# Optimization experiments

Hardware: AMD Instinct MI355X
Metric: run time of the kernel (lower is better)

Reference implementation:

```python
import jax, jax.numpy as jnp
import numpy as np

N_NODES = 100000
N_EDGES = 1600000
NUM_FEATURES = 128
HIDDEN = 128


def _linear_init(key, fan_in, fan_out):
    kw, kb = jax.random.split(key)
    bound = 1.0 / np.sqrt(fan_in)
    w = jax.random.uniform(kw, (fan_in, fan_out), jnp.float32, -bound, bound)
    b = jax.random.uniform(kb, (fan_out,), jnp.float32, -bound, bound)
    return w, b


def setup_inputs() -> dict:
    key = jax.random.key(0)
    ks = jax.random.split(key, 8)
    x = jax.random.normal(ks[0], (N_NODES, NUM_FEATURES), jnp.float32)
    edge_index = jax.random.randint(ks[1], (2, N_EDGES), 0, N_NODES, jnp.int64)
    w11, b11 = _linear_init(ks[2], NUM_FEATURES, HIDDEN)
    w12, b12 = _linear_init(ks[3], HIDDEN, HIDDEN)
    w21, b21 = _linear_init(ks[4], HIDDEN, HIDDEN)
    w22, b22 = _linear_init(ks[5], HIDDEN, HIDDEN)
    w31, b31 = _linear_init(ks[6], HIDDEN, HIDDEN)
    w32, b32 = _linear_init(ks[7], HIDDEN, 1)
    return {"x": x, "edge_index": edge_index,
            "w11": w11, "b11": b11, "w12": w12, "b12": b12,
            "w21": w21, "b21": b21, "w22": w22, "b22": b22,
            "w31": w31, "b31": b31, "w32": w32, "b32": b32}


def _gin_conv(x, src, dst, w1, b1, w2, b2):
    # GINConv (eps=0): h_i = MLP(x_i + sum_{j->i} x_j)
    agg = jax.ops.segment_sum(x[src], dst, num_segments=N_NODES)
    h = x + agg
    h = jax.nn.relu(h @ w1 + b1)
    return h @ w2 + b2


def reference(x, edge_index, w11, b11, w12, b12, w21, b21, w22, b22, w31, b31, w32, b32):
    src, dst = edge_index[0], edge_index[1]
    h = _gin_conv(x, src, dst, w11, b11, w12, b12)
    h = _gin_conv(h, src, dst, w21, b21, w22, b22)
    h = _gin_conv(h, src, dst, w31, b31, w32, b32)  # [N, 1]
    return h
```

## Files before the change

### kernel.cpp

```cpp
#include <hip/hip_runtime.h>

#define NN 100000
#define NE 1600000
#define F 128
#define NBUCK ((NN + 255) >> 8)
#define SCAT_BLOCKS 512
#define EPB (NE / SCAT_BLOCKS)
#define IDX_CAP 1536

typedef _Float16 f16x8 __attribute__((ext_vector_type(8)));
typedef float    f32x4 __attribute__((ext_vector_type(4)));
typedef unsigned short ushort8v __attribute__((ext_vector_type(8)));
typedef unsigned short ushort4v __attribute__((ext_vector_type(4)));

__device__ inline unsigned short f2h(float f) {
    _Float16 h = (_Float16)f;
    return __builtin_bit_cast(unsigned short, h);
}
__device__ inline float h2f(unsigned short u) {
    return (float)__builtin_bit_cast(_Float16, u);
}

__global__ __launch_bounds__(256) void k_bhist(const int* __restrict__ dst, int* __restrict__ bcnt) {
    __shared__ int sc[NBUCK];
    for (int i = threadIdx.x; i < NBUCK; i += 256) sc[i] = 0;
    __syncthreads();
    int stride = gridDim.x * 256;
    for (int e = blockIdx.x * 256 + threadIdx.x; e < NE; e += stride)
        atomicAdd(&sc[dst[e] >> 8], 1);
    __syncthreads();
    for (int i = threadIdx.x; i < NBUCK; i += 256) {
        int c = sc[i];
        if (c) atomicAdd(&bcnt[i], c);
    }
}

__global__ void k_bscan(const int* __restrict__ bcnt, int* __restrict__ bbase, int* __restrict__ bcur) {
    __shared__ int s[512];
    int t = threadIdx.x;
    int v = (t < NBUCK) ? bcnt[t] : 0;
    s[t] = v;
    __syncthreads();
    for (int off = 1; off < 512; off <<= 1) {
        int u = (t >= off) ? s[t - off] : 0;
        __syncthreads();
        s[t] += u;
        __syncthreads();
    }
    int excl = s[t] - v;
    if (t < NBUCK) { bbase[t] = excl; bcur[t] = excl; }
    if (t == 0) bbase[NBUCK] = NE;
}

__global__ __launch_bounds__(256) void k_scatterA(const int* __restrict__ src,
                                                  const int* __restrict__ dst,
                                                  int* __restrict__ bcur,
                                                  unsigned* __restrict__ scratch) {
    __shared__ uint2 sEdge[EPB];
    __shared__ int cnt[512];
    __shared__ int scn[512];
    __shared__ int cntB[512];
    __shared__ int gbase[512];
    __shared__ int ssum[256];

    const int tid = threadIdx.x;
    const int ebase = blockIdx.x * EPB;

#pragma unroll
    for (int i = tid; i < 512; i += 256) { cnt[i] = 0; cntB[i] = 0; }
    __syncthreads();

    for (int i = tid; i < EPB; i += 256) {
        int b = dst[ebase + i] >> 8;
        atomicAdd(&cnt[b], 1);
    }
    __syncthreads();

    int c0 = cnt[2 * tid], c1 = cnt[2 * tid + 1];
    ssum[tid] = c0 + c1;
    __syncthreads();
    for (int off = 1; off < 256; off <<= 1) {
        int v = (tid >= off) ? ssum[tid - off] : 0;
        __syncthreads();
        ssum[tid] += v;
        __syncthreads();
    }
    int texcl = (tid == 0) ? 0 : ssum[tid - 1];
    scn[2 * tid] = texcl;
    scn[2 * tid + 1] = texcl + c0;
#pragma unroll
    for (int i = tid; i < NBUCK; i += 256) {
        int c = cnt[i];
        gbase[i] = c ? atomicAdd(&bcur[i], c) : 0;
    }
    __syncthreads();

    for (int i = tid; i < EPB; i += 256) {
        int s = src[ebase + i], d = dst[ebase + i];
        int b = d >> 8;
        int rank = atomicAdd(&cntB[b], 1);
        sEdge[scn[b] + rank] = make_uint2((unsigned)s, (unsigned)d);
    }
    __syncthreads();

    for (int i = tid; i < EPB; i += 256) {
        uint2 ed = sEdge[i];
        int b = (int)(ed.y >> 8);
        unsigned w = ((ed.y & 255u) << 24) | ed.x;
        scratch[gbase[b] + (i - scn[b])] = w;
    }
}

__global__ __launch_bounds__(256) void k_fillB(const int* __restrict__ bbase,
                                               const unsigned* __restrict__ scratch,
                                               int* __restrict__ row_ptr,
                                               int* __restrict__ csr) {
    __shared__ int cnt[256];
    __shared__ int s[256];
    __shared__ int cur[256];
    int b = blockIdx.x;
    int base = bbase[b], end = bbase[b + 1];
    int t = threadIdx.x;
    cnt[t] = 0;
    __syncthreads();
    for (int i = base + t; i < end; i += 256)
        atomicAdd(&cnt[scratch[i] >> 24], 1);
    __syncthreads();
    int v = cnt[t];
    s[t] = v;
    __syncthreads();
    for (int off = 1; off < 256; off <<= 1) {
        int u = (t >= off) ? s[t - off] : 0;
        __syncthreads();
        s[t] += u;
        __syncthreads();
    }
    int excl = s[t] - v;
    int node = (b << 8) + t;
    if (node < NN) row_ptr[node] = base + excl;
    if (b == NBUCK - 1 && t == 0) row_ptr[NN] = NE;
    cur[t] = excl;
    __syncthreads();
    for (int i = base + t; i < end; i += 256) {
        unsigned w = scratch[i];
        int n = w >> 24;
        int p = atomicAdd(&cur[n], 1);
        csr[base + p] = (int)(w & 0xFFFFFFu);
    }
}

__global__ void k_x2h(const float* __restrict__ x, unsigned short* __restrict__ xh) {
    int idx = blockIdx.x * 256 + threadIdx.x;
    float4 v = ((const float4*)x)[idx];
    ushort4v h;
    h.x = f2h(v.x);
    h.y = f2h(v.y);
    h.z = f2h(v.z);
    h.w = f2h(v.w);
    ((ushort4v*)xh)[idx] = h;
}

struct WPack {
    const float* w[5];
    unsigned short* t[5];
};

__global__ void k_w2h(WPack p) {
    int which = blockIdx.x >> 6;
    int idx = (blockIdx.x & 63) * 256 + threadIdx.x;
    int n = idx >> 7, k = idx & 127;
    p.t[which][idx] = f2h(p.w[which][k * 128 + n]);
}

template <bool LOC>
__device__ __forceinline__ void accum_rows(float a[8], int st, int e,
                                           const int* __restrict__ sIdx,
                                           const int* __restrict__ gIdx,
                                           const unsigned short* __restrict__ G,
                                           int lofs) {
    int p = st;
    for (; p + 8 <= e; p += 8) {
        int j[8];
#pragma unroll
        for (int q = 0; q < 8; ++q) j[q] = LOC ? sIdx[p + q] : gIdx[p + q];
        ushort8v v[8];
#pragma unroll
        for (int q = 0; q < 8; ++q) v[q] = *(const ushort8v*)&G[(size_t)j[q] * F + lofs];
#pragma unroll
        for (int k = 0; k < 8; ++k) {
            float t0 = (h2f(v[0][k]) + h2f(v[1][k])) + (h2f(v[2][k]) + h2f(v[3][k]));
            float t1 = (h2f(v[4][k]) + h2f(v[5][k])) + (h2f(v[6][k]) + h2f(v[7][k]));
            a[k] += t0 + t1;
        }
    }
    if (p + 4 <= e) {
        int j[4];
#pragma unroll
        for (int q = 0; q < 4; ++q) j[q] = LOC ? sIdx[p + q] : gIdx[p + q];
        ushort8v v[4];
#pragma unroll
        for (int q = 0; q < 4; ++q) v[q] = *(const ushort8v*)&G[(size_t)j[q] * F + lofs];
#pragma unroll
        for (int k = 0; k < 8; ++k)
            a[k] += (h2f(v[0][k]) + h2f(v[1][k])) + (h2f(v[2][k]) + h2f(v[3][k]));
        p += 4;
    }
    if (p + 2 <= e) {
        int j0 = LOC ? sIdx[p] : gIdx[p];
        int j1 = LOC ? sIdx[p + 1] : gIdx[p + 1];
        ushort8v v0 = *(const ushort8v*)&G[(size_t)j0 * F + lofs];
        ushort8v v1 = *(const ushort8v*)&G[(size_t)j1 * F + lofs];
#pragma unroll
        for (int k = 0; k < 8; ++k) a[k] += h2f(v0[k]) + h2f(v1[k]);
        p += 2;
    }
    if (p < e) {
        int j0 = LOC ? sIdx[p] : gIdx[p];
        ushort8v v0 = *(const ushort8v*)&G[(size_t)j0 * F + lofs];
#pragma unroll
        for (int k = 0; k < 8; ++k) a[k] += h2f(v0[k]);
    }
}

template <int L3>
__global__ __launch_bounds__(256, 6) void k_layer(const unsigned short* __restrict__ G,
                                                  const int* __restrict__ row_ptr,
                                                  const int* __restrict__ csr,
                                                  const unsigned short* __restrict__ W1,
                                                  const float* __restrict__ b1,
                                                  const unsigned short* __restrict__ W2,
                                                  const float* __restrict__ b2,
                                                  const float* __restrict__ w32,
                                                  const float* __restrict__ b32,
                                                  unsigned short* __restrict__ H,
                                                  float* __restrict__ out) {
    __shared__ __align__(16) unsigned short sA[64 * 128];
    __shared__ int sRP[65];
    __shared__ int sIdx[IDX_CAP];

    const int tid = threadIdx.x;
    const int row0 = blockIdx.x * 64;
    const int cg   = tid >> 6;
    const int lane = tid & 63;
    const int m16  = lane & 15;
    const int quad = lane >> 4;

    if (tid < 65) {
        int n = row0 + tid;
        if (n > NN) n = NN;
        sRP[tid] = row_ptr[n];
    }
    __syncthreads();
    const int ibase = sRP[0];
    const int icnt  = sRP[64] - ibase;
    const int icap  = icnt < IDX_CAP ? icnt : IDX_CAP;
    for (int i = tid; i < icap; i += 256) sIdx[i] = csr[ibase + i];
    __syncthreads();

    {
        const int g = tid >> 4;
        const int l16 = tid & 15;
        const int lofs = l16 * 8;
#pragma unroll
        for (int it = 0; it < 4; ++it) {
            int r = it * 16 + g;
            int node = row0 + r;
            float a[8] = {};
            if (node < NN) {
                ushort8v sh = *(const ushort8v*)&G[(size_t)node * F + lofs];
#pragma unroll
                for (int k = 0; k < 8; ++k) a[k] = h2f(sh[k]);
                int st = sRP[r] - ibase, e = sRP[r + 1] - ibase;
                if (e <= icap)
                    accum_rows<true>(a, st, e, sIdx, csr + ibase, G, lofs);
                else
                    accum_rows<false>(a, st, e, sIdx, csr + ibase, G, lofs);
            }
            ushort8v o;
#pragma unroll
            for (int k = 0; k < 8; ++k) o[k] = f2h(a[k]);
            *(ushort8v*)&sA[r * 128 + ((l16 ^ (r & 15)) << 3)] = o;
        }
    }
    __syncthreads();

    f32x4 acc[4][2] = {};
#pragma unroll
    for (int ks = 0; ks < 4; ++ks) {
        f16x8 a[4];
#pragma unroll
        for (int rt = 0; rt < 4; ++rt) {
            int rowL = rt * 16 + m16;
            int u = ks * 4 + quad;
            a[rt] = *(const f16x8*)&sA[rowL * 128 + ((u ^ (rowL & 15)) << 3)];
        }
#pragma unroll
        for (int ct = 0; ct < 2; ++ct) {
            int widx = (cg * 32 + ct * 16 + m16) * 128 + ks * 32 + quad * 8;
            f16x8 b = *(const f16x8*)&W1[widx];
#pragma unroll
            for (int rt = 0; rt < 4; ++rt)
                acc[rt][ct] = __builtin_amdgcn_mfma_f32_16x16x32_f16(a[rt], b, acc[rt][ct], 0, 0, 0);
        }
    }

    if (L3) {
        float* psf = (float*)sA;
        __syncthreads();
#pragma unroll
        for (int rt = 0; rt < 4; ++rt) {
            float s[4] = {0.f, 0.f, 0.f, 0.f};
#pragma unroll
            for (int ct = 0; ct < 2; ++ct) {
                int col = cg * 32 + ct * 16 + m16;
                float bv = b1[col];
                float wv = w32[col];
#pragma unroll
                for (int i = 0; i < 4; ++i) {
                    float v = fmaxf(acc[rt][ct][i] + bv, 0.f);
                    s[i] += v * wv;
                }
            }
#pragma unroll
            for (int i = 0; i < 4; ++i) {
#pragma unroll
                for (int mask = 1; mask < 16; mask <<= 1)
                    s[i] += __shfl_xor(s[i], mask, 64);
            }
            if (m16 == 0) {
#pragma unroll
                for (int i = 0; i < 4; ++i) {
                    int rowL = rt * 16 + quad * 4 + i;
                    psf[rowL * 4 + cg] = s[i];
                }
            }
        }
        __syncthreads();
        if (tid < 64) {
            int row = row0 + tid;
            if (row < NN)
                out[row] = (psf[tid * 4] + psf[tid * 4 + 1]) + (psf[tid * 4 + 2] + psf[tid * 4 + 3]) + b32[0];
        }
        return;
    }

    __syncthreads();
#pragma unroll
    for (int rt = 0; rt < 4; ++rt) {
#pragma unroll
        for (int ct = 0; ct < 2; ++ct) {
            int col = cg * 32 + ct * 16 + m16;
            float bv = b1[col];
#pragma unroll
            for (int i = 0; i < 4; ++i) {
                int rL = rt * 16 + quad * 4 + i;
                float v = fmaxf(acc[rt][ct][i] + bv, 0.f);
                sA[rL * 128 + (((col >> 3) ^ (rL & 15)) << 3) + (col & 7)] = f2h(v);
            }
        }
    }
    __syncthreads();

    f32x4 acc2[4][2] = {};
#pragma unroll
    for (int ks = 0; ks < 4; ++ks) {
        f16x8 a[4];
#pragma unroll
        for (int rt = 0; rt < 4; ++rt) {
            int rowL = rt * 16 + m16;
            int u = ks * 4 + quad;
            a[rt] = *(const f16x8*)&sA[rowL * 128 + ((u ^ (rowL & 15)) << 3)];
        }
#pragma unroll
        for (int ct = 0; ct < 2; ++ct) {
            int widx = (cg * 32 + ct * 16 + m16) * 128 + ks * 32 + quad * 8;
            f16x8 b = *(const f16x8*)&W2[widx];
#pragma unroll
            for (int rt = 0; rt < 4; ++rt)
                acc2[rt][ct] = __builtin_amdgcn_mfma_f32_16x16x32_f16(a[rt], b, acc2[rt][ct], 0, 0, 0);
        }
    }

    __syncthreads();
#pragma unroll
    for (int rt = 0; rt < 4; ++rt) {
#pragma unroll
        for (int ct = 0; ct < 2; ++ct) {
            int col = cg * 32 + ct * 16 + m16;
            float bv = b2[col];
#pragma unroll
            for (int i = 0; i < 4; ++i) {
                int rL = rt * 16 + quad * 4 + i;
                float v = acc2[rt][ct][i] + bv;
                sA[rL * 128 + (((col >> 3) ^ (rL & 15)) << 3) + (col & 7)] = f2h(v);
            }
        }
    }
    __syncthreads();
    {
        ushort8v* go = (ushort8v*)(H + (size_t)row0 * F);
#pragma unroll
        for (int i = 0; i < 4; ++i) {
            int fg = i * 256 + tid;
            int r = fg >> 4, u = fg & 15;
            if (row0 + r < NN)
                go[fg] = *(const ushort8v*)&sA[r * 128 + ((u ^ (r & 15)) << 3)];
        }
    }
}

static inline size_t align256(size_t x) { return (x + 255) & ~(size_t)255; }

extern "C" void kernel_launch(void* const* d_in, const int* in_sizes, int n_in,
                              void* d_out, int out_size, void* d_ws, size_t ws_size,
                              hipStream_t stream) {
    const float* x   = (const float*)d_in[0];
    const int*   ei  = (const int*)d_in[1];
    const float* w11 = (const float*)d_in[2];
    const float* b11 = (const float*)d_in[3];
    const float* w12 = (const float*)d_in[4];
    const float* b12 = (const float*)d_in[5];
    const float* w21 = (const float*)d_in[6];
    const float* b21 = (const float*)d_in[7];
    const float* w22 = (const float*)d_in[8];
    const float* b22 = (const float*)d_in[9];
    const float* w31 = (const float*)d_in[10];
    const float* b31 = (const float*)d_in[11];
    const float* w32 = (const float*)d_in[12];
    const float* b32 = (const float*)d_in[13];
    float* out = (float*)d_out;

    const int* src = ei;
    const int* dst = ei + NE;

    char* ws = (char*)d_ws;
    size_t off = 0;
    unsigned short* Abuf = (unsigned short*)(ws + off); off += align256((size_t)NN * F * 2);
    unsigned short* Bbuf = (unsigned short*)(ws + off); off += align256((size_t)NN * F * 2);
    int* bcnt    = (int*)(ws + off); off += align256((size_t)NBUCK * 4);
    int* bbase   = (int*)(ws + off); off += align256((size_t)(NBUCK + 1) * 4);
    int* bcur    = (int*)(ws + off); off += align256((size_t)NBUCK * 4);
    int* row_ptr = (int*)(ws + off); off += align256((size_t)(NN + 1) * 4);
    int* csr     = (int*)(ws + off); off += align256((size_t)NE * 4);
    unsigned* scratch = (unsigned*)(ws + off); off += align256((size_t)NE * 4);
    unsigned short* wt[5];
    for (int i = 0; i < 5; ++i) {
        wt[i] = (unsigned short*)(ws + off); off += align256((size_t)128 * 128 * 2);
    }
    (void)ws_size;

    WPack wp;
    wp.w[0] = w11; wp.w[1] = w12; wp.w[2] = w21; wp.w[3] = w22; wp.w[4] = w31;
    for (int i = 0; i < 5; ++i) wp.t[i] = wt[i];
    k_w2h<<<320, 256, 0, stream>>>(wp);
    k_x2h<<<(NN * F / 4 + 255) / 256, 256, 0, stream>>>(x, Abuf);

    (void)hipMemsetAsync(bcnt, 0, (size_t)NBUCK * 4, stream);
    k_bhist<<<256, 256, 0, stream>>>(dst, bcnt);
    k_bscan<<<1, 512, 0, stream>>>(bcnt, bbase, bcur);
    k_scatterA<<<SCAT_BLOCKS, 256, 0, stream>>>(src, dst, bcur, scratch);
    k_fillB<<<NBUCK, 256, 0, stream>>>(bbase, scratch, row_ptr, csr);

    const int layerBlocks = (NN + 63) / 64;

    k_layer<0><<<layerBlocks, 256, 0, stream>>>(Abuf, row_ptr, csr,
                                                wt[0], b11, wt[1], b12,
                                                nullptr, nullptr, Bbuf, nullptr);
    k_layer<0><<<layerBlocks, 256, 0, stream>>>(Bbuf, row_ptr, csr,
                                                wt[2], b21, wt[3], b22,
                                                nullptr, nullptr, Abuf, nullptr);
    k_layer<1><<<layerBlocks, 256, 0, stream>>>(Abuf, row_ptr, csr,
                                                wt[4], b31, nullptr, nullptr,
                                                w32, b32, nullptr, out);
}
```

Baseline: 427.1 us.

## Split fused GIN layer into separate aggregation and MLP kernels

Each fused layer kernel is split into two kernels. The first, k_agg, does the neighbour aggregation with four blocks per 64-row tile, each block covering a 32-feature slice with one node per four threads, and writes the sum to a new fp16 AGG buffer. The second, k_mlp, loads AGG into shared memory and runs the MFMA MLP. The aim is more parallelism and occupancy for the latency-bound gather phase, kept apart from the register and LDS-heavy MLP. The cost is an extra round trip of the full aggregated feature matrix through global memory plus three more kernel launches, and the gather inner loop is narrowed from 8 to 4 loads in flight.

New measurement: 547.7 us. +28.2%, slower.

```diff
diff --git a/kernel.cpp b/kernel.cpp
--- a/kernel.cpp
+++ b/kernel.cpp
@@ -173,48 +173,26 @@
 }
 
 template <bool LOC>
-__device__ __forceinline__ void accum_rows(float a[8], int st, int e,
-                                           const int* __restrict__ sIdx,
-                                           const int* __restrict__ gIdx,
-                                           const unsigned short* __restrict__ G,
-                                           int lofs) {
+__device__ __forceinline__ void accum1(float a[8], int st, int e,
+                                       const int* __restrict__ sIdx,
+                                       const int* __restrict__ gIdx,
+                                       const unsigned short* __restrict__ G,
+                                       int lofs) {
     int p = st;
-    for (; p + 8 <= e; p += 8) {
-        int j[8];
-#pragma unroll
-        for (int q = 0; q < 8; ++q) j[q] = LOC ? sIdx[p + q] : gIdx[p + q];
-        ushort8v v[8];
-#pragma unroll
-        for (int q = 0; q < 8; ++q) v[q] = *(const ushort8v*)&G[(size_t)j[q] * F + lofs];
-#pragma unroll
-        for (int k = 0; k < 8; ++k) {
-            float t0 = (h2f(v[0][k]) + h2f(v[1][k])) + (h2f(v[2][k]) + h2f(v[3][k]));
-            float t1 = (h2f(v[4][k]) + h2f(v[5][k])) + (h2f(v[6][k]) + h2f(v[7][k]));
-            a[k] += t0 + t1;
-        }
-    }
-    if (p + 4 <= e) {
-        int j[4];
-#pragma unroll
-        for (int q = 0; q < 4; ++q) j[q] = LOC ? sIdx[p + q] : gIdx[p + q];
-        ushort8v v[4];
-#pragma unroll
-        for (int q = 0; q < 4; ++q) v[q] = *(const ushort8v*)&G[(size_t)j[q] * F + lofs];
-#pragma unroll
-        for (int k = 0; k < 8; ++k)
-            a[k] += (h2f(v[0][k]) + h2f(v[1][k])) + (h2f(v[2][k]) + h2f(v[3][k]));
-        p += 4;
-    }
-    if (p + 2 <= e) {
-        int j0 = LOC ? sIdx[p] : gIdx[p];
+    for (; p + 4 <= e; p += 4) {
+        int j0 = LOC ? sIdx[p]     : gIdx[p];
         int j1 = LOC ? sIdx[p + 1] : gIdx[p + 1];
+        int j2 = LOC ? sIdx[p + 2] : gIdx[p + 2];
+        int j3 = LOC ? sIdx[p + 3] : gIdx[p + 3];
         ushort8v v0 = *(const ushort8v*)&G[(size_t)j0 * F + lofs];
         ushort8v v1 = *(const ushort8v*)&G[(size_t)j1 * F + lofs];
-#pragma unroll
-        for (int k = 0; k < 8; ++k) a[k] += h2f(v0[k]) + h2f(v1[k]);
-        p += 2;
-    }
-    if (p < e) {
+        ushort8v v2 = *(const ushort8v*)&G[(size_t)j2 * F + lofs];
+        ushort8v v3 = *(const ushort8v*)&G[(size_t)j3 * F + lofs];
+#pragma unroll
+        for (int k = 0; k < 8; ++k)
+            a[k] += (h2f(v0[k]) + h2f(v1[k])) + (h2f(v2[k]) + h2f(v3[k]));
+    }
+    for (; p < e; ++p) {
         int j0 = LOC ? sIdx[p] : gIdx[p];
         ushort8v v0 = *(const ushort8v*)&G[(size_t)j0 * F + lofs];
 #pragma unroll
@@ -222,21 +200,64 @@
     }
 }
 
-template <int L3>
-__global__ __launch_bounds__(256, 6) void k_layer(const unsigned short* __restrict__ G,
-                                                  const int* __restrict__ row_ptr,
-                                                  const int* __restrict__ csr,
-                                                  const unsigned short* __restrict__ W1,
-                                                  const float* __restrict__ b1,
-                                                  const unsigned short* __restrict__ W2,
-                                                  const float* __restrict__ b2,
-                                                  const float* __restrict__ w32,
-                                                  const float* __restrict__ b32,
-                                                  unsigned short* __restrict__ H,
-                                                  float* __restrict__ out) {
-    __shared__ __align__(16) unsigned short sA[64 * 128];
+__global__ __launch_bounds__(256, 8) void k_agg(const unsigned short* __restrict__ G,
+                                                const int* __restrict__ row_ptr,
+                                                const int* __restrict__ csr,
+                                                unsigned short* __restrict__ AGG) {
     __shared__ int sRP[65];
     __shared__ int sIdx[IDX_CAP];
+
+    const int tid  = threadIdx.x;
+    const int tile = blockIdx.x >> 2;
+    const int c    = blockIdx.x & 3;
+    const int row0 = tile * 64;
+
+    if (tid < 65) {
+        int n = row0 + tid;
+        if (n > NN) n = NN;
+        sRP[tid] = row_ptr[n];
+    }
+    __syncthreads();
+    const int ibase = sRP[0];
+    const int icnt  = sRP[64] - ibase;
+    const int icap  = icnt < IDX_CAP ? icnt : IDX_CAP;
+    for (int i = tid; i < icap; i += 256) sIdx[i] = csr[ibase + i];
+    __syncthreads();
+
+    const int g    = tid >> 2;
+    const int l4   = tid & 3;
+    const int lofs = c * 32 + l4 * 8;
+    const int node = row0 + g;
+    if (node >= NN) return;
+
+    float a[8];
+    ushort8v sh = *(const ushort8v*)&G[(size_t)node * F + lofs];
+#pragma unroll
+    for (int k = 0; k < 8; ++k) a[k] = h2f(sh[k]);
+
+    int st = sRP[g] - ibase, e = sRP[g + 1] - ibase;
+    if (e <= icap)
+        accum1<true>(a, st, e, sIdx, csr + ibase, G, lofs);
+    else
+        accum1<false>(a, st, e, sIdx, csr + ibase, G, lofs);
+
+    ushort8v o;
+#pragma unroll
+    for (int k = 0; k < 8; ++k) o[k] = f2h(a[k]);
+    *(ushort8v*)&AGG[(size_t)node * F + lofs] = o;
+}
+
+template <int L3>
+__global__ __launch_bounds__(256, 6) void k_mlp(const unsigned short* __restrict__ AGG,
+                                                const unsigned short* __restrict__ W1,
+                                                const float* __restrict__ b1,
+                                                const unsigned short* __restrict__ W2,
+                                                const float* __restrict__ b2,
+                                                const float* __restrict__ w32,
+                                                const float* __restrict__ b32,
+                                                unsigned short* __restrict__ H,
+                                                float* __restrict__ out) {
+    __shared__ __align__(16) unsigned short sA[64 * 128];
 
     const int tid = threadIdx.x;
     const int row0 = blockIdx.x * 64;
@@ -245,42 +266,14 @@
     const int m16  = lane & 15;
     const int quad = lane >> 4;
 
-    if (tid < 65) {
-        int n = row0 + tid;
-        if (n > NN) n = NN;
-        sRP[tid] = row_ptr[n];
-    }
-    __syncthreads();
-    const int ibase = sRP[0];
-    const int icnt  = sRP[64] - ibase;
-    const int icap  = icnt < IDX_CAP ? icnt : IDX_CAP;
-    for (int i = tid; i < icap; i += 256) sIdx[i] = csr[ibase + i];
-    __syncthreads();
-
-    {
-        const int g = tid >> 4;
-        const int l16 = tid & 15;
-        const int lofs = l16 * 8;
-#pragma unroll
-        for (int it = 0; it < 4; ++it) {
-            int r = it * 16 + g;
-            int node = row0 + r;
-            float a[8] = {};
-            if (node < NN) {
-                ushort8v sh = *(const ushort8v*)&G[(size_t)node * F + lofs];
-#pragma unroll
-                for (int k = 0; k < 8; ++k) a[k] = h2f(sh[k]);
-                int st = sRP[r] - ibase, e = sRP[r + 1] - ibase;
-                if (e <= icap)
-                    accum_rows<true>(a, st, e, sIdx, csr + ibase, G, lofs);
-                else
-                    accum_rows<false>(a, st, e, sIdx, csr + ibase, G, lofs);
-            }
-            ushort8v o;
-#pragma unroll
-            for (int k = 0; k < 8; ++k) o[k] = f2h(a[k]);
-            *(ushort8v*)&sA[r * 128 + ((l16 ^ (r & 15)) << 3)] = o;
-        }
+#pragma unroll
+    for (int i = 0; i < 4; ++i) {
+        int fg = i * 256 + tid;
+        int r = fg >> 4, u = fg & 15;
+        ushort8v v = {};
+        if (row0 + r < NN)
+            v = *(const ushort8v*)&AGG[(size_t)row0 * F + fg * 8];
+        *(ushort8v*)&sA[r * 128 + ((u ^ (r & 15)) << 3)] = v;
     }
     __syncthreads();
 
@@ -437,6 +430,7 @@
     size_t off = 0;
     unsigned short* Abuf = (unsigned short*)(ws + off); off += align256((size_t)NN * F * 2);
     unsigned short* Bbuf = (unsigned short*)(ws + off); off += align256((size_t)NN * F * 2);
+    unsigned short* AGG  = (unsigned short*)(ws + off); off += align256((size_t)NN * F * 2);
     int* bcnt    = (int*)(ws + off); off += align256((size_t)NBUCK * 4);
     int* bbase   = (int*)(ws + off); off += align256((size_t)(NBUCK + 1) * 4);
     int* bcur    = (int*)(ws + off); off += align256((size_t)NBUCK * 4);
@@ -461,15 +455,16 @@
     k_scatterA<<<SCAT_BLOCKS, 256, 0, stream>>>(src, dst, bcur, scratch);
     k_fillB<<<NBUCK, 256, 0, stream>>>(bbase, scratch, row_ptr, csr);
 
-    const int layerBlocks = (NN + 63) / 64;
-
-    k_layer<0><<<layerBlocks, 256, 0, stream>>>(Abuf, row_ptr, csr,
-                                                wt[0], b11, wt[1], b12,
-                                                nullptr, nullptr, Bbuf, nullptr);
-    k_layer<0><<<layerBlocks, 256, 0, stream>>>(Bbuf, row_ptr, csr,
-                                                wt[2], b21, wt[3], b22,
-                                                nullptr, nullptr, Abuf, nullptr);
-    k_layer<1><<<layerBlocks, 256, 0, stream>>>(Abuf, row_ptr, csr,
-                                                wt[4], b31, nullptr, nullptr,
-                                                w32, b32, nullptr, out);
-}
+    const int tiles = (NN + 63) / 64;
+    const int aggBlocks = tiles * 4;
+
+    k_agg<<<aggBlocks, 256, 0, stream>>>(Abuf, row_ptr, csr, AGG);
+    k_mlp<0><<<tiles, 256, 0, stream>>>(AGG, wt[0], b11, wt[1], b12,
+                                        nullptr, nullptr, Bbuf, nullptr);
+    k_agg<<<aggBlocks, 256, 0, stream>>>(Bbuf, row_ptr, csr, AGG);
+    k_mlp<0><<<tiles, 256, 0, stream>>>(AGG, wt[2], b21, wt[3], b22,
+                                        nullptr, nullptr, Abuf, nullptr);
+    k_agg<<<aggBlocks, 256, 0, stream>>>(Abuf, row_ptr, csr, AGG);
+    k_mlp<1><<<tiles, 256, 0, stream>>>(AGG, wt[4], b31, nullptr, nullptr,
+                                        w32, b32, nullptr, out);
+}
```
